# Kernel tuning notes

Hardware: AMD Instinct MI355X
Metric: run time of the kernel (lower is better)

## Reference

```python
import jax, jax.numpy as jnp
import numpy as np

NB_HEAD = 16
DIM_PER_HEAD = 64
EMB = 1024
B, SQ, SK = 4, 2048, 2048


def setup_inputs() -> dict:
    key = jax.random.key(0)
    ks = jax.random.split(key, 8)
    scale = 1.0 / np.sqrt(EMB)
    return {
        "hidden_state_query": jax.random.normal(ks[0], (B, SQ, EMB), jnp.float32),
        "hidden_state_key": jax.random.normal(ks[1], (B, SK, EMB), jnp.float32),
        "hidden_state_value": jax.random.normal(ks[2], (B, SK, EMB), jnp.float32),
        "attention_mask": jax.random.randint(ks[3], (B, SQ, SK), 0, 2).astype(bool),
        "Wq": jax.random.uniform(ks[4], (NB_HEAD * DIM_PER_HEAD, EMB), jnp.float32, -scale, scale),
        "Wk": jax.random.uniform(ks[5], (NB_HEAD * DIM_PER_HEAD, EMB), jnp.float32, -scale, scale),
        "Wv": jax.random.uniform(ks[6], (NB_HEAD * DIM_PER_HEAD, EMB), jnp.float32, -scale, scale),
        "Wo": jax.random.uniform(ks[7], (EMB, NB_HEAD * DIM_PER_HEAD), jnp.float32, -scale, scale),
    }


def reference(hidden_state_query, hidden_state_key, hidden_state_value,
              attention_mask, Wq, Wk, Wv, Wo):
    bs, sq, _ = hidden_state_query.shape
    sk = hidden_state_key.shape[1]
    # projections (nn.Linear without bias: x @ W.T)
    q = (hidden_state_query @ Wq.T).reshape(bs, sq, NB_HEAD, DIM_PER_HEAD).transpose(0, 2, 1, 3)
    k = (hidden_state_key @ Wk.T).reshape(bs, sk, NB_HEAD, DIM_PER_HEAD).transpose(0, 2, 1, 3)
    v = (hidden_state_value @ Wv.T).reshape(bs, sk, NB_HEAD, DIM_PER_HEAD).transpose(0, 2, 1, 3)
    scores = jnp.einsum('bhqd,bhkd->bhqk', q, k) / jnp.sqrt(jnp.asarray(DIM_PER_HEAD, q.dtype))
    attn = jax.nn.softmax(scores, axis=-1)
    # POST-softmax zero masking (True -> 0), broadcast over heads; no renormalization
    attn = jnp.where(attention_mask[:, None, :, :], jnp.asarray(0.0, attn.dtype), attn)
    ctx = jnp.einsum('bhqk,bhkd->bhqd', attn, v)  # [B,H,Sq,Dh]
    ctx = ctx.transpose(0, 2, 1, 3).reshape(bs, sq, NB_HEAD * DIM_PER_HEAD)
    return ctx @ Wo.T + hidden_state_query
```

## Files before the change

### kernel.cpp

```cpp
#include <hip/hip_runtime.h>
#include <hip/hip_bf16.h>
#include <stdint.h>

typedef __bf16 bf16_t;
typedef bf16_t bf16x2 __attribute__((ext_vector_type(2)));
typedef bf16_t bf16x8 __attribute__((ext_vector_type(8)));
typedef float  f32x4  __attribute__((ext_vector_type(4)));
typedef float  f32x16 __attribute__((ext_vector_type(16)));
typedef unsigned uint2v __attribute__((ext_vector_type(2)));

#define NB_HEAD 16
#define DH      64
#define EMB     1024
#define BATCH   4
#define SEQ     2048
#define NTOK    (BATCH*SEQ)

#define QSCALE 0.1803368801111204f

__device__ __forceinline__ void gload_lds16(const void* g, void* l) {
  __builtin_amdgcn_global_load_lds(
      (const __attribute__((address_space(1))) void*)g,
      (__attribute__((address_space(3))) void*)l, 16, 0, 0);
}

__device__ __forceinline__ uint32_t pkbf(float a, float b) {
  bf16x2 v = { (bf16_t)a, (bf16_t)b };
  return __builtin_bit_cast(uint32_t, v);
}

__device__ __forceinline__ void cvt8_body(const float* __restrict__ in,
                                          bf16_t* __restrict__ out, int i) {
  const float4* p = reinterpret_cast<const float4*>(in) + (size_t)i * 2;
  float4 a = p[0], b = p[1];
  uint4 r;
  r.x = pkbf(a.x, a.y); r.y = pkbf(a.z, a.w);
  r.z = pkbf(b.x, b.y); r.w = pkbf(b.z, b.w);
  reinterpret_cast<uint4*>(out)[i] = r;
}

__device__ __forceinline__ void mkand_body(const uint8_t* __restrict__ m,
                                           uint16_t* __restrict__ out, int i) {
  uint2 v = reinterpret_cast<const uint2*>(m)[i];
  uint4 r;
  uint32_t lo = v.x, hi = v.y;
  uint16_t e[8];
#pragma unroll
  for (int j = 0; j < 4; j++) e[j]     = (uint16_t)(((lo >> (8 * j)) & 0xFF) - 1);
#pragma unroll
  for (int j = 0; j < 4; j++) e[4 + j] = (uint16_t)(((hi >> (8 * j)) & 0xFF) - 1);
  r.x = (uint32_t)e[0] | ((uint32_t)e[1] << 16);
  r.y = (uint32_t)e[2] | ((uint32_t)e[3] << 16);
  r.z = (uint32_t)e[4] | ((uint32_t)e[5] << 16);
  r.w = (uint32_t)e[6] | ((uint32_t)e[7] << 16);
  reinterpret_cast<uint4*>(out)[i] = r;
}

__global__ void __launch_bounds__(256)
prep(const float* __restrict__ hq, const float* __restrict__ hk,
     const float* __restrict__ hv, const float* __restrict__ Wq,
     const float* __restrict__ Wk, const float* __restrict__ Wv,
     const float* __restrict__ Wo,
     bf16_t* hq_b, bf16_t* hk_b, bf16_t* hv_b,
     bf16_t* Wq_b, bf16_t* Wk_b, bf16_t* Wv_b, bf16_t* Wo_b,
     const uint8_t* __restrict__ mask, uint16_t* __restrict__ mand) {
  const int bid = blockIdx.x;
  if (bid < 12288) {
    const int seg = bid >> 12;
    const float* src = seg == 0 ? hq : seg == 1 ? hk : hv;
    bf16_t*      dst = seg == 0 ? hq_b : seg == 1 ? hk_b : hv_b;
    cvt8_body(src, dst, (bid & 4095) * 256 + (int)threadIdx.x);
  } else if (bid < 14336) {
    const int sb = bid - 12288;
    const int seg = sb >> 9;
    const float* src = seg == 0 ? Wq : seg == 1 ? Wk : seg == 2 ? Wv : Wo;
    bf16_t*      dst = seg == 0 ? Wq_b : seg == 1 ? Wk_b : seg == 2 ? Wv_b : Wo_b;
    cvt8_body(src, dst, (sb & 511) * 256 + (int)threadIdx.x);
  } else {
    mkand_body(mask, mand, (bid - 14336) * 256 + (int)threadIdx.x);
  }
}

__global__ void __launch_bounds__(256)
mkand(const uint8_t* __restrict__ m, uint16_t* __restrict__ out) {
  mkand_body(m, out, blockIdx.x * 256 + (int)threadIdx.x);
}

#define BM 128
#define BN 128
#define BKT 64

template<int EPI>
__global__ void __launch_bounds__(256, 2)
gemm_bt(const bf16_t* __restrict__ A, const bf16_t* __restrict__ Bw,
        bf16_t* __restrict__ Cb, float* __restrict__ Cf,
        const float* __restrict__ resid, float qscale) {
  __shared__ bf16_t As[2][BM * BKT];
  __shared__ bf16_t Bs[2][BN * BKT];
  const int K = EMB, N = EMB;
  const int t    = threadIdx.x;
  const int lane = t & 63, w = t >> 6;
  const int wr = w >> 1, wc = w & 1;
  const int l15 = lane & 15, l4 = lane >> 4;

  const int lin = blockIdx.x + 8 * blockIdx.y;
  const int nl  = (lin & 7) * 64 + (lin >> 3);
  const int rowBase = (nl >> 3) * BM, colBase = (nl & 7) * BN;

  f32x4 acc[4][4];
#pragma unroll
  for (int i = 0; i < 4; i++)
#pragma unroll
    for (int j = 0; j < 4; j++) acc[i][j] = f32x4{0.f, 0.f, 0.f, 0.f};

  const int lin16 = w * 1024 + lane * 16;

#pragma unroll
  for (int i = 0; i < 4; ++i) {
    int off  = i * 4096 + lin16;
    int row  = off >> 7, colb = off & 127;
    gload_lds16((const char*)A  + (((size_t)(rowBase + row)) * K) * 2 + colb, (char*)As[0] + off);
    gload_lds16((const char*)Bw + (((size_t)(colBase + row)) * K) * 2 + colb, (char*)Bs[0] + off);
  }
  __syncthreads();

  int cur = 0;
  for (int k0 = 0; k0 < K; k0 += BKT) {
    if (k0 + BKT < K) {
      const int nb = cur ^ 1;
#pragma unroll
      for (int i = 0; i < 4; ++i) {
        int off  = i * 4096 + lin16;
        int row  = off >> 7, colb = off & 127;
        gload_lds16((const char*)A  + (((size_t)(rowBase + row)) * K + k0 + BKT) * 2 + colb, (char*)As[nb] + off);
        gload_lds16((const char*)Bw + (((size_t)(colBase + row)) * K + k0 + BKT) * 2 + colb, (char*)Bs[nb] + off);
      }
    }
#pragma unroll
    for (int kc = 0; kc < 2; ++kc) {
      bf16x8 af[4], bfb[4];
#pragma unroll
      for (int mi = 0; mi < 4; mi++)
        af[mi] = *reinterpret_cast<const bf16x8*>(
            &As[cur][(wr * 64 + mi * 16 + l15) * BKT + kc * 32 + l4 * 8]);
#pragma unroll
      for (int ni = 0; ni < 4; ni++)
        bfb[ni] = *reinterpret_cast<const bf16x8*>(
            &Bs[cur][(wc * 64 + ni * 16 + l15) * BKT + kc * 32 + l4 * 8]);
      __builtin_amdgcn_s_setprio(1);
#pragma unroll
      for (int mi = 0; mi < 4; mi++)
#pragma unroll
        for (int ni = 0; ni < 4; ni++)
          acc[mi][ni] = __builtin_amdgcn_mfma_f32_16x16x32_bf16(
              af[mi], bfb[ni], acc[mi][ni], 0, 0, 0);
      __builtin_amdgcn_s_setprio(0);
    }
    __syncthreads();
    cur ^= 1;
  }

#pragma unroll
  for (int mi = 0; mi < 4; mi++) {
#pragma unroll
    for (int ni = 0; ni < 4; ni++) {
      const int m0 = rowBase + wr * 64 + mi * 16 + l4 * 4;
      const int n  = colBase + wc * 64 + ni * 16 + l15;
      if (EPI == 1) {
        size_t base = ((size_t)((m0 >> 11) * 1024 + n)) * 2048 + (m0 & 2047);
        uint2 st;
        st.x = pkbf(acc[mi][ni][0], acc[mi][ni][1]);
        st.y = pkbf(acc[mi][ni][2], acc[mi][ni][3]);
        *reinterpret_cast<uint2*>(Cb + base) = st;
      } else {
#pragma unroll
        for (int r = 0; r < 4; r++) {
          int m = m0 + r;
          float v = acc[mi][ni][r];
          if (EPI == 0) {
            Cb[(size_t)m * N + n] = (bf16_t)(v * qscale);
          } else if (EPI == 3) {
            Cb[(((size_t)((m >> 11) * 16 + (n >> 6))) * 2048 + (m & 2047)) * 64 + (n & 63)] = (bf16_t)v;
          } else {
            Cf[(size_t)m * N + n] = v + resid[(size_t)m * N + n];
          }
        }
      }
    }
  }
}

#define KVB 128

__global__ void __launch_bounds__(512, 4)
attn32(const bf16_t* __restrict__ Qb, const bf16_t* __restrict__ Kh,
       const bf16_t* __restrict__ Vt, const uint16_t* __restrict__ Mand,
       bf16_t* __restrict__ ctx) {
  __shared__ __align__(16) bf16_t Ks[2][KVB * 64];
  __shared__ __align__(16) bf16_t Vs[2][64 * KVB];

  const int t = threadIdx.x, lane = t & 63, wid = t >> 6;
  const int q = lane & 31, hi = lane >> 5;

  const int lin = blockIdx.x + 8 * (blockIdx.y + 16 * blockIdx.z);
  const int nl  = (lin & 7) * 64 + (lin >> 3);
  const int bx = nl & 7, h = (nl >> 3) & 15, b = nl >> 7;

  const int q0 = bx * 256 + wid * 32;
  const int qrow = b * SEQ + q0 + q;

  const int srow8  = t >> 3;
  const int scol8  = ((t & 7) ^ ((t >> 3) & 7)) * 16;
  const int srow16 = t >> 4;
  const int scol16 = (((t & 15) ^ ((t >> 4) & 7)) & 15) * 16;
  const char* kg = (const char*)(Kh + ((size_t)(b * NB_HEAD + h)) * SEQ * DH);
  const char* vg = (const char*)(Vt + ((size_t)(b * NB_HEAD + h)) * DH * SEQ);

  const bf16_t* qp = Qb + (size_t)qrow * EMB + h * DH + hi * 8;
  bf16x8 qf[4];
#pragma unroll
  for (int d = 0; d < 4; d++) qf[d] = *reinterpret_cast<const bf16x8*>(qp + d * 16);

  bf16x8 ones;
#pragma unroll
  for (int i = 0; i < 8; i++) ones[i] = (bf16_t)1.0f;

  f32x16 o0 = {0}, o1 = {0}, sacc = {0};
  const uint16_t* mbase = Mand + (size_t)qrow * SEQ;
  const int qx = (q & 7) << 4;

  gload_lds16(kg + (size_t)srow8 * 128 + scol8,                 (char*)Ks[0] + t * 16);
  gload_lds16(kg + (size_t)(64 + srow8) * 128 + scol8,          (char*)Ks[0] + 8192 + t * 16);
  gload_lds16(vg + (size_t)srow16 * 4096 + scol16,              (char*)Vs[0] + t * 16);
  gload_lds16(vg + (size_t)(32 + srow16) * 4096 + scol16,       (char*)Vs[0] + 8192 + t * 16);
  __syncthreads();

  int cur = 0;
#pragma unroll 1
  for (int kb = 0; kb < SEQ; kb += KVB) {
    if (kb + KVB < SEQ) {
      const int nb = cur ^ 1;
      const size_t kO = (size_t)(kb + KVB) * 128;
      const size_t vO = (size_t)(kb + KVB) * 2;
      gload_lds16(kg + kO + (size_t)srow8 * 128 + scol8,           (char*)Ks[nb] + t * 16);
      gload_lds16(kg + kO + (size_t)(64 + srow8) * 128 + scol8,    (char*)Ks[nb] + 8192 + t * 16);
      gload_lds16(vg + vO + (size_t)srow16 * 4096 + scol16,        (char*)Vs[nb] + t * 16);
      gload_lds16(vg + vO + (size_t)(32 + srow16) * 4096 + scol16, (char*)Vs[nb] + 8192 + t * 16);
    }

#pragma unroll
    for (int hh = 0; hh < 2; hh++) {
      const char* kls = (const char*)Ks[cur] + hh * 8192;
      f32x16 p0 = {0}, p1 = {0};
      __builtin_amdgcn_s_setprio(1);
#pragma unroll
      for (int dsl = 0; dsl < 4; dsl++) {
        const int cb = (dsl * 32 + hi * 16) ^ qx;
        bf16x8 kf0 = *reinterpret_cast<const bf16x8*>(kls + q * 128 + cb);
        bf16x8 kf1 = *reinterpret_cast<const bf16x8*>(kls + (32 + q) * 128 + cb);
        p0 = __builtin_amdgcn_mfma_f32_32x32x16_bf16(kf0, qf[dsl], p0, 0, 0, 0);
        p1 = __builtin_amdgcn_mfma_f32_32x32x16_bf16(kf1, qf[dsl], p1, 0, 0, 0);
      }
      __builtin_amdgcn_s_setprio(0);

      uint4 mv[4];
#pragma unroll
      for (int ks = 0; ks < 4; ks++)
        mv[ks] = *reinterpret_cast<const uint4*>(mbase + kb + 64 * hh + 16 * ks + 8 * hi);

      const char* vls = (const char*)Vs[cur];

#pragma unroll
      for (int i = 0; i < 16; i++) p0[i] = __builtin_amdgcn_exp2f(p0[i]);

#pragma unroll
      for (int half = 0; half < 2; half++) {
        if (half == 1) {
#pragma unroll
          for (int i = 0; i < 16; i++) p1[i] = __builtin_amdgcn_exp2f(p1[i]);
        }
        const f32x16& ph = half ? p1 : p0;
#pragma unroll
        for (int kss = 0; kss < 2; kss++) {
          const int ks = half * 2 + kss;
          const int s8 = kss * 8;
          uint32_t a0 = pkbf(ph[s8+0], ph[s8+1]), a1 = pkbf(ph[s8+2], ph[s8+3]);
          uint32_t a2 = pkbf(ph[s8+4], ph[s8+5]), a3 = pkbf(ph[s8+6], ph[s8+7]);
          uint2v s02 = __builtin_amdgcn_permlane32_swap(a0, a2, false, false);
          uint2v s13 = __builtin_amdgcn_permlane32_swap(a1, a3, false, false);
          uint4 fr;
          fr.x = s02[0]; fr.y = s13[0]; fr.z = s02[1]; fr.w = s13[1];
          bf16x8 pa_raw = __builtin_bit_cast(bf16x8, fr);
          sacc = __builtin_amdgcn_mfma_f32_32x32x16_bf16(ones, pa_raw, sacc, 0, 0, 0);
          fr.x &= mv[ks].x; fr.y &= mv[ks].y; fr.z &= mv[ks].z; fr.w &= mv[ks].w;
          bf16x8 pa = __builtin_bit_cast(bf16x8, fr);
          const int cbv = (hh * 128 + ks * 32 + hi * 16) ^ qx;
          bf16x8 vf0 = *reinterpret_cast<const bf16x8*>(vls + q * 256 + cbv);
          bf16x8 vf1 = *reinterpret_cast<const bf16x8*>(vls + (32 + q) * 256 + cbv);
          __builtin_amdgcn_s_setprio(1);
          o0 = __builtin_amdgcn_mfma_f32_32x32x16_bf16(vf0, pa, o0, 0, 0, 0);
          o1 = __builtin_amdgcn_mfma_f32_32x32x16_bf16(vf1, pa, o1, 0, 0, 0);
          __builtin_amdgcn_s_setprio(0);
        }
      }
    }

    __syncthreads();
    cur ^= 1;
  }

  float inv = 1.0f / sacc[0];
  bf16_t* cp = ctx + (size_t)qrow * EMB + h * DH;
#pragma unroll
  for (int g = 0; g < 4; g++) {
    uint2 st;
    st.x = pkbf(o0[4*g+0] * inv, o0[4*g+1] * inv);
    st.y = pkbf(o0[4*g+2] * inv, o0[4*g+3] * inv);
    *reinterpret_cast<uint2*>(cp + 8 * g + 4 * hi) = st;
    st.x = pkbf(o1[4*g+0] * inv, o1[4*g+1] * inv);
    st.y = pkbf(o1[4*g+2] * inv, o1[4*g+3] * inv);
    *reinterpret_cast<uint2*>(cp + 32 + 8 * g + 4 * hi) = st;
  }
}

extern "C" void kernel_launch(void* const* d_in, const int* in_sizes, int n_in,
                              void* d_out, int out_size, void* d_ws, size_t ws_size,
                              hipStream_t stream) {
  const float*   hq   = (const float*)d_in[0];
  const float*   hk   = (const float*)d_in[1];
  const float*   hv   = (const float*)d_in[2];
  const uint8_t* mask = (const uint8_t*)d_in[3];
  const float*   Wq   = (const float*)d_in[4];
  const float*   Wk   = (const float*)d_in[5];
  const float*   Wv   = (const float*)d_in[6];
  const float*   Wo   = (const float*)d_in[7];
  float* out = (float*)d_out;

  char* ws = (char*)d_ws;
  const size_t SZ_H = (size_t)NTOK * EMB * 2;
  const size_t SZ_W = (size_t)EMB * EMB * 2;
  bf16_t* hq_b = (bf16_t*)(ws + 0 * SZ_H);
  bf16_t* hk_b = (bf16_t*)(ws + 1 * SZ_H);
  bf16_t* hv_b = (bf16_t*)(ws + 2 * SZ_H);
  bf16_t* Qb   = (bf16_t*)(ws + 3 * SZ_H);
  bf16_t* Kh   = (bf16_t*)(ws + 4 * SZ_H);
  bf16_t* Vt   = (bf16_t*)(ws + 5 * SZ_H);
  bf16_t* ctx  = (bf16_t*)(ws + 6 * SZ_H);
  bf16_t* Wq_b = (bf16_t*)(ws + 7 * SZ_H + 0 * SZ_W);
  bf16_t* Wk_b = (bf16_t*)(ws + 7 * SZ_H + 1 * SZ_W);
  bf16_t* Wv_b = (bf16_t*)(ws + 7 * SZ_H + 2 * SZ_W);
  bf16_t* Wo_b = (bf16_t*)(ws + 7 * SZ_H + 3 * SZ_W);

  const size_t MAND_OFF = 7 * SZ_H + 4 * SZ_W;
  const size_t MAND_SZ  = (size_t)BATCH * SEQ * SEQ * 2;
  const bool bigws = ws_size >= MAND_OFF + MAND_SZ;
  uint16_t* Mand = bigws ? (uint16_t*)(ws + MAND_OFF) : (uint16_t*)ws;

  prep<<<bigws ? 22528 : 14336, 256, 0, stream>>>(
      hq, hk, hv, Wq, Wk, Wv, Wo,
      hq_b, hk_b, hv_b, Wq_b, Wk_b, Wv_b, Wo_b, mask, Mand);

  dim3 ggrid(EMB / BN, NTOK / BM);
  gemm_bt<0><<<ggrid, 256, 0, stream>>>(hq_b, Wq_b, Qb, nullptr, nullptr, QSCALE);
  gemm_bt<3><<<ggrid, 256, 0, stream>>>(hk_b, Wk_b, Kh, nullptr, nullptr, 1.0f);
  gemm_bt<1><<<ggrid, 256, 0, stream>>>(hv_b, Wv_b, Vt, nullptr, nullptr, 1.0f);

  if (!bigws) mkand<<<8192, 256, 0, stream>>>(mask, Mand);

  attn32<<<dim3(SEQ / 256, NB_HEAD, BATCH), 512, 0, stream>>>(Qb, Kh, Vt, Mand, ctx);

  gemm_bt<2><<<ggrid, 256, 0, stream>>>(ctx, Wo_b, nullptr, out, hq, 1.0f);
}
```

Baseline: 255.3 us.

## Use one barrier with vmcnt waits per iteration, compute softmax row sums on VALU

In both the projection GEMM and the attention loop, the two __syncthreads per K/V tile are replaced by a single s_barrier at the top of each iteration. It is preceded by an explicit s_waitcnt that waits only for the current buffer's global-to-LDS loads, so the prefetch of the next tile can stay in flight. The softmax denominator is no longer accumulated with an extra MFMA against a ones vector. Each lane instead sums its exp2 values on the VALU, and a cross-half __shfl_xor combines them into a running float. The risk is a write-after-read hazard: a fast wave may issue prefetch into the buffer that slower waves are still reading from the previous iteration, and the sum now uses fp32 values rather than bf16-rounded ones.

New measurement: 388.6 us. 1.52x slower.

```diff
diff --git a/kernel.cpp b/kernel.cpp
--- a/kernel.cpp
+++ b/kernel.cpp
@@ -122,7 +122,6 @@
     gload_lds16((const char*)A  + (((size_t)(rowBase + row)) * K) * 2 + colb, (char*)As[0] + off);
     gload_lds16((const char*)Bw + (((size_t)(colBase + row)) * K) * 2 + colb, (char*)Bs[0] + off);
   }
-  __syncthreads();
 
   int cur = 0;
   for (int k0 = 0; k0 < K; k0 += BKT) {
@@ -135,7 +134,13 @@
         gload_lds16((const char*)A  + (((size_t)(rowBase + row)) * K + k0 + BKT) * 2 + colb, (char*)As[nb] + off);
         gload_lds16((const char*)Bw + (((size_t)(colBase + row)) * K + k0 + BKT) * 2 + colb, (char*)Bs[nb] + off);
       }
-    }
+      asm volatile("s_waitcnt vmcnt(8)" ::: "memory");
+    } else {
+      asm volatile("s_waitcnt vmcnt(0)" ::: "memory");
+    }
+    __builtin_amdgcn_s_barrier();
+    __builtin_amdgcn_sched_barrier(0);
+
 #pragma unroll
     for (int kc = 0; kc < 2; ++kc) {
       bf16x8 af[4], bfb[4];
@@ -156,7 +161,6 @@
               af[mi], bfb[ni], acc[mi][ni], 0, 0, 0);
       __builtin_amdgcn_s_setprio(0);
     }
-    __syncthreads();
     cur ^= 1;
   }
 
@@ -221,11 +225,8 @@
 #pragma unroll
   for (int d = 0; d < 4; d++) qf[d] = *reinterpret_cast<const bf16x8*>(qp + d * 16);
 
-  bf16x8 ones;
-#pragma unroll
-  for (int i = 0; i < 8; i++) ones[i] = (bf16_t)1.0f;
-
-  f32x16 o0 = {0}, o1 = {0}, sacc = {0};
+  f32x16 o0 = {0}, o1 = {0};
+  float lrun = 0.f;
   const uint16_t* mbase = Mand + (size_t)qrow * SEQ;
   const int qx = (q & 7) << 4;
 
@@ -233,7 +234,6 @@
   gload_lds16(kg + (size_t)(64 + srow8) * 128 + scol8,          (char*)Ks[0] + 8192 + t * 16);
   gload_lds16(vg + (size_t)srow16 * 4096 + scol16,              (char*)Vs[0] + t * 16);
   gload_lds16(vg + (size_t)(32 + srow16) * 4096 + scol16,       (char*)Vs[0] + 8192 + t * 16);
-  __syncthreads();
 
   int cur = 0;
 #pragma unroll 1
@@ -246,7 +246,12 @@
       gload_lds16(kg + kO + (size_t)(64 + srow8) * 128 + scol8,    (char*)Ks[nb] + 8192 + t * 16);
       gload_lds16(vg + vO + (size_t)srow16 * 4096 + scol16,        (char*)Vs[nb] + t * 16);
       gload_lds16(vg + vO + (size_t)(32 + srow16) * 4096 + scol16, (char*)Vs[nb] + 8192 + t * 16);
-    }
+      asm volatile("s_waitcnt vmcnt(4)" ::: "memory");
+    } else {
+      asm volatile("s_waitcnt vmcnt(0)" ::: "memory");
+    }
+    __builtin_amdgcn_s_barrier();
+    __builtin_amdgcn_sched_barrier(0);
 
 #pragma unroll
     for (int hh = 0; hh < 2; hh++) {
@@ -270,14 +275,15 @@
 
       const char* vls = (const char*)Vs[cur];
 
-#pragma unroll
-      for (int i = 0; i < 16; i++) p0[i] = __builtin_amdgcn_exp2f(p0[i]);
+      float ps = 0.f;
+#pragma unroll
+      for (int i = 0; i < 16; i++) { p0[i] = __builtin_amdgcn_exp2f(p0[i]); ps += p0[i]; }
 
 #pragma unroll
       for (int half = 0; half < 2; half++) {
         if (half == 1) {
 #pragma unroll
-          for (int i = 0; i < 16; i++) p1[i] = __builtin_amdgcn_exp2f(p1[i]);
+          for (int i = 0; i < 16; i++) { p1[i] = __builtin_amdgcn_exp2f(p1[i]); ps += p1[i]; }
         }
         const f32x16& ph = half ? p1 : p0;
 #pragma unroll
@@ -290,8 +296,6 @@
           uint2v s13 = __builtin_amdgcn_permlane32_swap(a1, a3, false, false);
           uint4 fr;
           fr.x = s02[0]; fr.y = s13[0]; fr.z = s02[1]; fr.w = s13[1];
-          bf16x8 pa_raw = __builtin_bit_cast(bf16x8, fr);
-          sacc = __builtin_amdgcn_mfma_f32_32x32x16_bf16(ones, pa_raw, sacc, 0, 0, 0);
           fr.x &= mv[ks].x; fr.y &= mv[ks].y; fr.z &= mv[ks].z; fr.w &= mv[ks].w;
           bf16x8 pa = __builtin_bit_cast(bf16x8, fr);
           const int cbv = (hh * 128 + ks * 32 + hi * 16) ^ qx;
@@ -303,13 +307,13 @@
           __builtin_amdgcn_s_setprio(0);
         }
       }
-    }
-
-    __syncthreads();
+      ps += __shfl_xor(ps, 32);
+      lrun += ps;
+    }
     cur ^= 1;
   }
 
-  float inv = 1.0f / sacc[0];
+  float inv = 1.0f / lrun;
   bf16_t* cp = ctx + (size_t)qrow * EMB + h * DH;
 #pragma unroll
   for (int g = 0; g < 4; g++) {
```
